# Kernel tuning notes

Measured on AMD Instinct MI355X. Metric: run time of the kernel, lower is better.

The kernel has to match this reference:

```python
import jax, jax.numpy as jnp
import numpy as np
from jax import lax

HID = 128


def setup_inputs() -> dict:
    key = jax.random.key(0)
    ks = jax.random.split(key, 14)
    B, T, D_IN, OUT, L = 256, 300, 700, 20, 4
    x = jax.random.normal(ks[0], (B, T, D_IN), jnp.float32)
    w_in = jax.random.normal(ks[1], (D_IN, HID), jnp.float32) / np.sqrt(D_IN).astype(np.float32)
    b_in = jnp.zeros((HID,), jnp.float32)
    A_w = jax.random.normal(ks[2], (L, HID, HID), jnp.float32) / np.sqrt(HID).astype(np.float32)
    # sparse recurrent mask: keep-prob 0.3 (dropout=0.7), no self-connections
    mask = (jax.random.uniform(ks[3], (L, HID, HID)) > 0.7).astype(jnp.float32) * (1.0 - jnp.eye(HID, dtype=jnp.float32))
    A_w = A_w * mask
    A_b = jax.random.normal(ks[4], (L, HID), jnp.float32) * 0.01
    fc_w = jax.random.normal(ks[5], (L, HID, HID), jnp.float32) / np.sqrt(HID).astype(np.float32)
    fc_b = jnp.zeros((L, HID), jnp.float32)
    w_out = jax.random.normal(ks[6], (L * HID, OUT), jnp.float32) / np.sqrt(L * HID).astype(np.float32)
    b_out = jnp.zeros((OUT,), jnp.float32)
    thr = jax.random.uniform(ks[7], (HID,), jnp.float32) * 0.5
    decay = jax.random.uniform(ks[8], (HID,), jnp.float32) * 0.5
    rst = jax.random.uniform(ks[9], (HID,), jnp.float32) * 0.05
    mem0 = jax.random.uniform(ks[10], (L, B, HID), jnp.float32) * 0.1  # torch uniform_(0, 0.1)
    return dict(x=x, w_in=w_in, b_in=b_in, A_w=A_w, A_b=A_b, fc_w=fc_w, fc_b=fc_b,
                w_out=w_out, b_out=b_out, thr=thr, decay=decay, rst=rst, mem0=mem0)


def reference(x, w_in, b_in, A_w, A_b, fc_w, fc_b, w_out, b_out, thr, decay, rst, mem0):
    B, T, _ = x.shape
    # fixed input projection (fc_in frozen in original) -> [B,T,HID]
    inp = jnp.einsum('btd,dh->bth', x, w_in) + b_in
    # parallel mode: each reservoir drive depends only on input_t -> precompute all timesteps
    xs = jnp.einsum('bth,lhk->ltbk', inp, A_w) + A_b[:, None, None, :]  # [L,T,B,HID]
    xs = xs.transpose(1, 0, 2, 3)  # [T,L,B,HID]

    def step(carry, x_t):
        mem, spk = carry
        mem = rst * spk + mem * decay * (1.0 - spk) + x_t
        spike = (mem - thr > 0).astype(mem.dtype)
        return (mem, spike), (mem, spike)

    spk0 = jnp.zeros_like(mem0)
    _, (mems, spks) = lax.scan(step, (mem0, spk0), xs)  # each [T,L,B,HID]

    rates = spks.mean(axis=0)  # [L,B,HID] == sum_spk / time_step
    outs = jax.nn.relu(jnp.einsum('lbh,lhk->lbk', rates, fc_w) + fc_b[:, None, :])
    cat = jnp.concatenate([outs[0], outs[1], outs[2], outs[3]], axis=1)  # [B,4*HID]
    out = cat @ w_out + b_out  # [B,OUT]

    hid4_mem = jnp.concatenate([mem0[3][:, None, :], mems[:, 3].transpose(1, 0, 2)], axis=1)  # [B,T+1,HID]
    hid4_spk = jnp.concatenate([jnp.zeros((B, 1, HID), x.dtype), spks[:, 3].transpose(1, 0, 2)], axis=1)
    A_norm = jnp.sum(jnp.abs(A_w))
    return out, hid4_mem, hid4_spk, A_norm
```

## Files before the change

kernel.cpp:

```cpp
#include <hip/hip_runtime.h>

#define HID_   128
#define BB_    256
#define TT_    300
#define DIN_   700
#define LL_    4
#define NOUT_  20
#define NROWS_ (BB_*TT_)

#define OUT_OFF   0
#define HMEM_OFF  5120
#define HSPK_OFF  (5120 + 256*301*128)
#define ANORM_OFF (5120 + 2*256*301*128)

typedef __attribute__((ext_vector_type(8))) short  bfrag;
typedef __attribute__((ext_vector_type(4))) float  f32x4;

__device__ __forceinline__ unsigned short f2bf(float f) {
    unsigned int u = __float_as_uint(f);
    return (unsigned short)((u + 0x7fffu + ((u >> 16) & 1u)) >> 16);
}
__device__ __forceinline__ float bf2f(unsigned short h) {
    return __uint_as_float(((unsigned int)h) << 16);
}
__device__ __forceinline__ void split2(float v, unsigned short& hi, unsigned short& lo) {
    hi = f2bf(v);
    lo = f2bf(v - bf2f(hi));
}

__global__ __launch_bounds__(256, 2)
void k1_mfma(const float* __restrict__ x, const float* __restrict__ w,
             const float* __restrict__ bin, float* __restrict__ inp)
{
    __shared__ unsigned short whi[128 * 40];
    __shared__ unsigned short wlo[128 * 40];

    const int tid  = threadIdx.x;
    const int wave = tid >> 6;
    const int lane = tid & 63;
    const int l15  = lane & 15;
    const int kg   = lane >> 4;
    const long m0  = (long)blockIdx.x * 64 + wave * 16;
    const long arow = m0 + l15;

    f32x4 acc[8];
#pragma unroll
    for (int nt = 0; nt < 8; ++nt) {
        const float bv = bin[nt * 16 + l15];
        acc[nt] = (f32x4){bv, bv, bv, bv};
    }

    for (int ks = 0; ks < 22; ++ks) {
        const int k0 = ks * 32;
        const int lim = (700 - k0) * 128;
        const float* __restrict__ wsrc = w + (long)k0 * 128;
#pragma unroll
        for (int j = 0; j < 16; ++j) {
            const int i = tid + j * 256;
            const int kk = i >> 7, nn = i & 127;
            float v = (i < lim) ? wsrc[i] : 0.f;
            unsigned short hi, lo;
            split2(v, hi, lo);
            whi[nn * 40 + kk] = hi;
            wlo[nn * 40 + kk] = lo;
        }
        __syncthreads();

        bfrag ahi, alo;
        const int kbase = k0 + kg * 8;
        const float* __restrict__ xr = x + arow * (long)DIN_ + kbase;
        if (kbase + 7 < 700) {
            const float4 p0 = *(const float4*)(xr);
            const float4 p1 = *(const float4*)(xr + 4);
            float vv[8] = {p0.x, p0.y, p0.z, p0.w, p1.x, p1.y, p1.z, p1.w};
#pragma unroll
            for (int j = 0; j < 8; ++j) {
                unsigned short hi, lo; split2(vv[j], hi, lo);
                ahi[j] = (short)hi; alo[j] = (short)lo;
            }
        } else {
#pragma unroll
            for (int j = 0; j < 8; ++j) {
                float v = (kbase + j < 700) ? xr[j] : 0.f;
                unsigned short hi, lo; split2(v, hi, lo);
                ahi[j] = (short)hi; alo[j] = (short)lo;
            }
        }

#pragma unroll
        for (int nt = 0; nt < 8; ++nt) {
            const int boff = (nt * 16 + l15) * 40 + kg * 8;
            const bfrag bhi = *(const bfrag*)&whi[boff];
            const bfrag blo = *(const bfrag*)&wlo[boff];
            acc[nt] = __builtin_amdgcn_mfma_f32_16x16x32_bf16(ahi, bhi, acc[nt], 0, 0, 0);
            acc[nt] = __builtin_amdgcn_mfma_f32_16x16x32_bf16(ahi, blo, acc[nt], 0, 0, 0);
            acc[nt] = __builtin_amdgcn_mfma_f32_16x16x32_bf16(alo, bhi, acc[nt], 0, 0, 0);
        }
        __syncthreads();
    }

#pragma unroll
    for (int nt = 0; nt < 8; ++nt) {
        const int col = nt * 16 + l15;
#pragma unroll
        for (int reg = 0; reg < 4; ++reg)
            inp[(m0 + kg * 4 + reg) * (long)HID_ + col] = acc[nt][reg];
    }
}

__global__ __launch_bounds__(256, 2)
void k2_mfma(const float* __restrict__ inp, const float* __restrict__ Aw,
             const float* __restrict__ Ab, float* __restrict__ xs,
             int lsel, long lstride)
{
    __shared__ unsigned short ahiS[128 * 72];
    __shared__ unsigned short aloS[128 * 72];

    const int tid  = threadIdx.x;
    const int wave = tid >> 6;
    const int lane = tid & 63;
    const int l15  = lane & 15;
    const int kg   = lane >> 4;
    const int l    = (lsel >= 0) ? lsel : (int)blockIdx.y;
    const long m0  = (long)blockIdx.x * 64 + wave * 16;
    const long arow = m0 + l15;
    const long lbase = (lsel >= 0) ? 0 : (long)l * lstride;

    f32x4 acc[8];
#pragma unroll
    for (int nt = 0; nt < 8; ++nt) {
        const float bv = Ab[l * 128 + nt * 16 + l15];
        acc[nt] = (f32x4){bv, bv, bv, bv};
    }

    const float* __restrict__ Al = Aw + (long)l * 128 * 128;

    for (int kc = 0; kc < 2; ++kc) {
        const float* __restrict__ asrc = Al + (long)kc * 64 * 128;
#pragma unroll
        for (int j = 0; j < 32; ++j) {
            const int i = tid + j * 256;
            const int kk = i >> 7, nn = i & 127;
            unsigned short hi, lo;
            split2(asrc[i], hi, lo);
            ahiS[nn * 72 + kk] = hi;
            aloS[nn * 72 + kk] = lo;
        }
        __syncthreads();

#pragma unroll
        for (int ks = 0; ks < 2; ++ks) {
            const int k0 = kc * 64 + ks * 32;
            bfrag ahi, alo;
            const float* __restrict__ ir = inp + arow * (long)HID_ + k0 + kg * 8;
            const float4 p0 = *(const float4*)(ir);
            const float4 p1 = *(const float4*)(ir + 4);
            float vv[8] = {p0.x, p0.y, p0.z, p0.w, p1.x, p1.y, p1.z, p1.w};
#pragma unroll
            for (int j = 0; j < 8; ++j) {
                unsigned short hi, lo; split2(vv[j], hi, lo);
                ahi[j] = (short)hi; alo[j] = (short)lo;
            }

#pragma unroll
            for (int nt = 0; nt < 8; ++nt) {
                const int boff = (nt * 16 + l15) * 72 + ks * 32 + kg * 8;
                const bfrag bhi = *(const bfrag*)&ahiS[boff];
                const bfrag blo = *(const bfrag*)&aloS[boff];
                acc[nt] = __builtin_amdgcn_mfma_f32_16x16x32_bf16(ahi, bhi, acc[nt], 0, 0, 0);
                acc[nt] = __builtin_amdgcn_mfma_f32_16x16x32_bf16(ahi, blo, acc[nt], 0, 0, 0);
                acc[nt] = __builtin_amdgcn_mfma_f32_16x16x32_bf16(alo, bhi, acc[nt], 0, 0, 0);
            }
        }
        __syncthreads();
    }

#pragma unroll
    for (int nt = 0; nt < 8; ++nt) {
        const int col = nt * 16 + l15;
#pragma unroll
        for (int reg = 0; reg < 4; ++reg)
            xs[(lbase + m0 + kg * 4 + reg) * (long)HID_ + col] = acc[nt][reg];
    }
}

__global__ __launch_bounds__(128, 4)
void k3_scan_split(const float* __restrict__ xs, const float* __restrict__ thr,
                   const float* __restrict__ dec, const float* __restrict__ rstv,
                   const float* __restrict__ mem0, float* __restrict__ rates,
                   float* __restrict__ omem, float* __restrict__ ospk,
                   int lsel, long lstride)
{
    const int h = threadIdx.x;
    int l, b;
    if (lsel >= 0) { l = lsel; b = blockIdx.x; }
    else           { l = blockIdx.x >> 8; b = blockIdx.x & 255; }

    const float th = thr[h];
    const float dc = dec[h];
    const float rs = rstv[h];

    float mem = mem0[((long)l * 256 + b) * 128 + h];
    float spk = 0.f;
    float cnt = 0.f;

    const bool last = (l == 3);
    float* __restrict__ om = omem + (long)b * 301 * 128 + h;
    float* __restrict__ os = ospk + (long)b * 301 * 128 + h;
    if (last) { om[0] = mem; os[0] = 0.f; }

    const float* __restrict__ p =
        xs + ((lsel >= 0 ? 0L : (long)l * lstride) + (long)b * TT_) * HID_ + h;

    for (int t0 = 0; t0 < TT_; t0 += 20) {
        float v[20];
#pragma unroll
        for (int j = 0; j < 20; ++j) v[j] = p[(long)(t0 + j) * HID_];
#pragma unroll
        for (int j = 0; j < 20; ++j) {
            mem = rs * spk + mem * dc * (1.f - spk) + v[j];
            spk = (mem - th > 0.f) ? 1.f : 0.f;
            cnt += spk;
            if (last) {
                om[(long)(t0 + j + 1) * 128] = mem;
                os[(long)(t0 + j + 1) * 128] = spk;
            }
        }
    }

    rates[((long)l * 256 + b) * 128 + h] = cnt * (1.f / 300.f);
}

__global__ __launch_bounds__(128, 2)
void k3_fused(const float* __restrict__ inp, const float* __restrict__ Aw,
              const float* __restrict__ Ab, const float* __restrict__ thr,
              const float* __restrict__ dec, const float* __restrict__ rstv,
              const float* __restrict__ mem0, float* __restrict__ rates,
              float* __restrict__ omem, float* __restrict__ ospk)
{
    const int h = threadIdx.x;
    const int l = blockIdx.x & 3;
    const int b = blockIdx.x >> 2;

    float a[128];
#pragma unroll
    for (int k = 0; k < 128; ++k)
        a[k] = Aw[((long)l * 128 + k) * 128 + h];

    const float ab = Ab[l * 128 + h];
    const float th = thr[h];
    const float dc = dec[h];
    const float rs = rstv[h];

    float mem = mem0[((long)l * 256 + b) * 128 + h];
    float spk = 0.f, cnt = 0.f;

    const bool last = (l == 3);
    float* __restrict__ om = omem + (long)b * 301 * 128 + h;
    float* __restrict__ os = ospk + (long)b * 301 * 128 + h;
    if (last) { om[0] = mem; os[0] = 0.f; }

    const float* __restrict__ ip = inp + (long)b * 300 * 128;

    for (int t = 0; t < 300; ++t) {
        float acc = ab;
#pragma unroll
        for (int k = 0; k < 128; ++k)
            acc = fmaf(ip[k], a[k], acc);
        ip += 128;
        mem = rs * spk + mem * dc * (1.f - spk) + acc;
        spk = (mem - th > 0.f) ? 1.f : 0.f;
        cnt += spk;
        if (last) {
            om[(long)(t + 1) * 128] = mem;
            os[(long)(t + 1) * 128] = spk;
        }
    }
    rates[((long)l * 256 + b) * 128 + h] = cnt * (1.f / 300.f);
}

__global__ __launch_bounds__(256)
void k4_head(const float* __restrict__ rates, const float* __restrict__ fcw,
             const float* __restrict__ fcb, const float* __restrict__ wout,
             const float* __restrict__ bout, float* __restrict__ out)
{
    __shared__ float cat[512];
    const int b = blockIdx.x;
    const int tid = threadIdx.x;

    for (int c = tid; c < 512; c += 256) {
        const int l = c >> 7;
        const int k = c & 127;
        float s = fcb[l * 128 + k];
        const float* __restrict__ rp = rates + ((long)l * 256 + b) * 128;
        const float* __restrict__ wp = fcw + (long)l * 128 * 128 + k;
#pragma unroll 8
        for (int hh = 0; hh < 128; ++hh)
            s = fmaf(rp[hh], wp[(long)hh * 128], s);
        cat[c] = s > 0.f ? s : 0.f;
    }
    __syncthreads();

    if (tid < NOUT_) {
        float s = bout[tid];
#pragma unroll 8
        for (int c = 0; c < 512; ++c)
            s = fmaf(cat[c], wout[(long)c * NOUT_ + tid], s);
        out[(long)b * NOUT_ + tid] = s;
    }
}

__global__ __launch_bounds__(256)
void k5_anorm(const float* __restrict__ Aw, float* __restrict__ out)
{
    __shared__ float red[256];
    const int tid = threadIdx.x;
    float s = 0.f;
    for (int i = tid; i < LL_ * 128 * 128; i += 256)
        s += fabsf(Aw[i]);
    red[tid] = s;
    __syncthreads();
#pragma unroll
    for (int st = 128; st > 0; st >>= 1) {
        if (tid < st) red[tid] += red[tid + st];
        __syncthreads();
    }
    if (tid == 0) out[0] = red[0];
}

extern "C" void kernel_launch(void* const* d_in, const int* in_sizes, int n_in,
                              void* d_out, int out_size, void* d_ws, size_t ws_size,
                              hipStream_t stream)
{
    const float* x    = (const float*)d_in[0];
    const float* w_in = (const float*)d_in[1];
    const float* b_in = (const float*)d_in[2];
    const float* A_w  = (const float*)d_in[3];
    const float* A_b  = (const float*)d_in[4];
    const float* fc_w = (const float*)d_in[5];
    const float* fc_b = (const float*)d_in[6];
    const float* w_out= (const float*)d_in[7];
    const float* b_out= (const float*)d_in[8];
    const float* thr  = (const float*)d_in[9];
    const float* dec  = (const float*)d_in[10];
    const float* rst  = (const float*)d_in[11];
    const float* mem0 = (const float*)d_in[12];

    float* out = (float*)d_out;
    float* ws  = (float*)d_ws;

    const long INP_ELTS = (long)NROWS_ * HID_;
    const long XS_FULL  = 4L * NROWS_ * HID_;
    const long RATES    = 4L * 256 * 128;

    float* inp = ws;

    k1_mfma<<<1200, 256, 0, stream>>>(x, w_in, b_in, inp);

    const size_t need_full = (size_t)(INP_ELTS + XS_FULL + RATES) * 4;
    const size_t need_perl = (size_t)(INP_ELTS + INP_ELTS + RATES) * 4;

    if (ws_size >= need_full) {
        float* xs    = ws + INP_ELTS;
        float* rates = xs + XS_FULL;
        k2_mfma<<<dim3(1200, 4), 256, 0, stream>>>(inp, A_w, A_b, xs, -1, (long)NROWS_);
        k3_scan_split<<<1024, 128, 0, stream>>>(xs, thr, dec, rst, mem0, rates,
                                                out + HMEM_OFF, out + HSPK_OFF,
                                                -1, (long)NROWS_);
        k4_head<<<256, 256, 0, stream>>>(rates, fc_w, fc_b, w_out, b_out, out + OUT_OFF);
    } else if (ws_size >= need_perl) {
        float* xs    = ws + INP_ELTS;
        float* rates = xs + INP_ELTS;
        for (int l = 0; l < 4; ++l) {
            k2_mfma<<<dim3(1200, 1), 256, 0, stream>>>(inp, A_w, A_b, xs, l, 0L);
            k3_scan_split<<<256, 128, 0, stream>>>(xs, thr, dec, rst, mem0, rates,
                                                   out + HMEM_OFF, out + HSPK_OFF,
                                                   l, 0L);
        }
        k4_head<<<256, 256, 0, stream>>>(rates, fc_w, fc_b, w_out, b_out, out + OUT_OFF);
    } else {
        float* rates = ws + INP_ELTS;
        k3_fused<<<1024, 128, 0, stream>>>(inp, A_w, A_b, thr, dec, rst, mem0,
                                           rates, out + HMEM_OFF, out + HSPK_OFF);
        k4_head<<<256, 256, 0, stream>>>(rates, fc_w, fc_b, w_out, b_out, out + OUT_OFF);
    }

    k5_anorm<<<1, 256, 0, stream>>>(A_w, out + ANORM_OFF);
}
```

Before: 738.8 us.

## Presplit weights into bf16 hi/lo fragment layout and use register-tiled GEMMs

Adds a prepass kernel that splits w_in and A_w into bf16 hi/lo pairs, stored in MFMA fragment order in the workspace. New input-projection and reservoir-drive kernels then read B fragments straight from global memory instead of staging and splitting them in LDS. Each wave now handles 32 rows, and the drive kernel loops over all four layers so each block reuses its input tile. The aim is to cut repeated weight splitting and LDS traffic, at the cost of an extra launch, more workspace, and heavier register pressure.

```diff
diff --git a/kernel.cpp b/kernel.cpp
--- a/kernel.cpp
+++ b/kernel.cpp
@@ -13,6 +13,10 @@
 #define HSPK_OFF  (5120 + 256*301*128)
 #define ANORM_OFF (5120 + 2*256*301*128)
 
+#define W1ELTS (22*4096)
+#define A2ELTS (4*4*4096)
+#define PRESPLIT_FLOATS ((2*W1ELTS + 2*A2ELTS)/2)
+
 typedef __attribute__((ext_vector_type(8))) short  bfrag;
 typedef __attribute__((ext_vector_type(4))) float  f32x4;
 
@@ -26,6 +30,175 @@
 __device__ __forceinline__ void split2(float v, unsigned short& hi, unsigned short& lo) {
     hi = f2bf(v);
     lo = f2bf(v - bf2f(hi));
+}
+
+__global__ __launch_bounds__(256)
+void k0_presplit(const float* __restrict__ w, const float* __restrict__ Aw,
+                 unsigned short* __restrict__ w1hi, unsigned short* __restrict__ w1lo,
+                 unsigned short* __restrict__ a2hi, unsigned short* __restrict__ a2lo)
+{
+    const int f = blockIdx.x * 256 + threadIdx.x;
+    if (f < W1ELTS) {
+        const int ks = f >> 12, r = f & 4095;
+        const int nt = r >> 9, l15 = (r >> 5) & 15, kk = r & 31;
+        const int k = ks * 32 + kk, n = nt * 16 + l15;
+        const float v = (k < DIN_) ? w[(long)k * HID_ + n] : 0.f;
+        unsigned short hi, lo; split2(v, hi, lo);
+        w1hi[f] = hi; w1lo[f] = lo;
+    } else {
+        const int g = f - W1ELTS;
+        const int l = g >> 14, r2 = g & 16383;
+        const int ks = r2 >> 12, r = r2 & 4095;
+        const int nt = r >> 9, l15 = (r >> 5) & 15, kk = r & 31;
+        const int k = ks * 32 + kk, n = nt * 16 + l15;
+        const float v = Aw[(long)l * 16384 + (long)k * HID_ + n];
+        unsigned short hi, lo; split2(v, hi, lo);
+        a2hi[g] = hi; a2lo[g] = lo;
+    }
+}
+
+__global__ __launch_bounds__(256, 2)
+void k1_reg(const float* __restrict__ x,
+            const unsigned short* __restrict__ whi,
+            const unsigned short* __restrict__ wlo,
+            const float* __restrict__ bin, float* __restrict__ inp)
+{
+    const int tid  = threadIdx.x;
+    const int wave = tid >> 6;
+    const int lane = tid & 63;
+    const int l15  = lane & 15;
+    const int kg   = lane >> 4;
+    const long m0  = (long)blockIdx.x * 128 + wave * 32;
+
+    f32x4 acc[2][8];
+#pragma unroll
+    for (int nt = 0; nt < 8; ++nt) {
+        const float bv = bin[nt * 16 + l15];
+        acc[0][nt] = (f32x4){bv, bv, bv, bv};
+        acc[1][nt] = (f32x4){bv, bv, bv, bv};
+    }
+
+    const int foff = l15 * 32 + kg * 8;
+
+    for (int ks = 0; ks < 22; ++ks) {
+        const int kbase = ks * 32 + kg * 8;
+
+        bfrag ahi[2], alo[2];
+#pragma unroll
+        for (int m = 0; m < 2; ++m) {
+            const float* __restrict__ xr = x + (m0 + m * 16 + l15) * (long)DIN_ + kbase;
+            if (kbase + 7 < DIN_) {
+                const float4 p0 = *(const float4*)(xr);
+                const float4 p1 = *(const float4*)(xr + 4);
+                float vv[8] = {p0.x, p0.y, p0.z, p0.w, p1.x, p1.y, p1.z, p1.w};
+#pragma unroll
+                for (int j = 0; j < 8; ++j) {
+                    unsigned short hi, lo; split2(vv[j], hi, lo);
+                    ahi[m][j] = (short)hi; alo[m][j] = (short)lo;
+                }
+            } else {
+#pragma unroll
+                for (int j = 0; j < 8; ++j) {
+                    float v = (kbase + j < DIN_) ? xr[j] : 0.f;
+                    unsigned short hi, lo; split2(v, hi, lo);
+                    ahi[m][j] = (short)hi; alo[m][j] = (short)lo;
+                }
+            }
+        }
+
+        const unsigned short* __restrict__ wh = whi + (long)ks * 4096 + foff;
+        const unsigned short* __restrict__ wl = wlo + (long)ks * 4096 + foff;
+#pragma unroll
+        for (int nt = 0; nt < 8; ++nt) {
+            const bfrag bhi = *(const bfrag*)(wh + nt * 512);
+            const bfrag blo = *(const bfrag*)(wl + nt * 512);
+#pragma unroll
+            for (int m = 0; m < 2; ++m) {
+                acc[m][nt] = __builtin_amdgcn_mfma_f32_16x16x32_bf16(ahi[m], bhi, acc[m][nt], 0, 0, 0);
+                acc[m][nt] = __builtin_amdgcn_mfma_f32_16x16x32_bf16(ahi[m], blo, acc[m][nt], 0, 0, 0);
+                acc[m][nt] = __builtin_amdgcn_mfma_f32_16x16x32_bf16(alo[m], bhi, acc[m][nt], 0, 0, 0);
+            }
+        }
+    }
+
+#pragma unroll
+    for (int m = 0; m < 2; ++m)
+#pragma unroll
+        for (int nt = 0; nt < 8; ++nt) {
+            const int col = nt * 16 + l15;
+#pragma unroll
+            for (int reg = 0; reg < 4; ++reg)
+                inp[(m0 + m * 16 + kg * 4 + reg) * (long)HID_ + col] = acc[m][nt][reg];
+        }
+}
+
+__global__ __launch_bounds__(256, 2)
+void k2_reg(const float* __restrict__ inp,
+            const unsigned short* __restrict__ ahiP,
+            const unsigned short* __restrict__ aloP,
+            const float* __restrict__ Ab, float* __restrict__ xs)
+{
+    const int tid  = threadIdx.x;
+    const int wave = tid >> 6;
+    const int lane = tid & 63;
+    const int l15  = lane & 15;
+    const int kg   = lane >> 4;
+    const long m0  = (long)blockIdx.x * 128 + wave * 32;
+    const int foff = l15 * 32 + kg * 8;
+
+    for (int l = 0; l < 4; ++l) {
+        f32x4 acc[2][8];
+#pragma unroll
+        for (int nt = 0; nt < 8; ++nt) {
+            const float bv = Ab[l * HID_ + nt * 16 + l15];
+            acc[0][nt] = (f32x4){bv, bv, bv, bv};
+            acc[1][nt] = (f32x4){bv, bv, bv, bv};
+        }
+
+        const unsigned short* __restrict__ ph = ahiP + (long)l * 16384;
+        const unsigned short* __restrict__ pl = aloP + (long)l * 16384;
+
+#pragma unroll
+        for (int ks = 0; ks < 4; ++ks) {
+            bfrag xhi[2], xlo[2];
+#pragma unroll
+            for (int m = 0; m < 2; ++m) {
+                const float* __restrict__ ir = inp + (m0 + m * 16 + l15) * (long)HID_ + ks * 32 + kg * 8;
+                const float4 p0 = *(const float4*)(ir);
+                const float4 p1 = *(const float4*)(ir + 4);
+                float vv[8] = {p0.x, p0.y, p0.z, p0.w, p1.x, p1.y, p1.z, p1.w};
+#pragma unroll
+                for (int j = 0; j < 8; ++j) {
+                    unsigned short hi, lo; split2(vv[j], hi, lo);
+                    xhi[m][j] = (short)hi; xlo[m][j] = (short)lo;
+                }
+            }
+
+            const unsigned short* __restrict__ bh = ph + ks * 4096 + foff;
+            const unsigned short* __restrict__ bl = pl + ks * 4096 + foff;
+#pragma unroll
+            for (int nt = 0; nt < 8; ++nt) {
+                const bfrag bhi = *(const bfrag*)(bh + nt * 512);
+                const bfrag blo = *(const bfrag*)(bl + nt * 512);
+#pragma unroll
+                for (int m = 0; m < 2; ++m) {
+                    acc[m][nt] = __builtin_amdgcn_mfma_f32_16x16x32_bf16(xhi[m], bhi, acc[m][nt], 0, 0, 0);
+                    acc[m][nt] = __builtin_amdgcn_mfma_f32_16x16x32_bf16(xhi[m], blo, acc[m][nt], 0, 0, 0);
+                    acc[m][nt] = __builtin_amdgcn_mfma_f32_16x16x32_bf16(xlo[m], bhi, acc[m][nt], 0, 0, 0);
+                }
+            }
+        }
+
+#pragma unroll
+        for (int m = 0; m < 2; ++m)
+#pragma unroll
+            for (int nt = 0; nt < 8; ++nt) {
+                const int col = nt * 16 + l15;
+#pragma unroll
+                for (int reg = 0; reg < 4; ++reg)
+                    xs[((long)l * NROWS_ + m0 + m * 16 + kg * 4 + reg) * (long)HID_ + col] = acc[m][nt][reg];
+            }
+    }
 }
 
 __global__ __launch_bounds__(256, 2)
@@ -353,24 +526,42 @@
     const long XS_FULL  = 4L * NROWS_ * HID_;
     const long RATES    = 4L * 256 * 128;
 
-    float* inp = ws;
-
-    k1_mfma<<<1200, 256, 0, stream>>>(x, w_in, b_in, inp);
-
+    const size_t need_v2   = (size_t)(PRESPLIT_FLOATS + INP_ELTS + XS_FULL + RATES) * 4;
     const size_t need_full = (size_t)(INP_ELTS + XS_FULL + RATES) * 4;
     const size_t need_perl = (size_t)(INP_ELTS + INP_ELTS + RATES) * 4;
 
-    if (ws_size >= need_full) {
+    if (ws_size >= need_v2) {
+        unsigned short* us   = (unsigned short*)ws;
+        unsigned short* w1hi = us;
+        unsigned short* w1lo = us + W1ELTS;
+        unsigned short* a2hi = us + 2 * W1ELTS;
+        unsigned short* a2lo = us + 2 * W1ELTS + A2ELTS;
+        float* inp   = ws + PRESPLIT_FLOATS;
+        float* xs    = inp + INP_ELTS;
+        float* rates = xs + XS_FULL;
+
+        k0_presplit<<<608, 256, 0, stream>>>(w_in, A_w, w1hi, w1lo, a2hi, a2lo);
+        k1_reg<<<600, 256, 0, stream>>>(x, w1hi, w1lo, b_in, inp);
+        k2_reg<<<600, 256, 0, stream>>>(inp, a2hi, a2lo, A_b, xs);
+        k3_scan_split<<<1024, 128, 0, stream>>>(xs, thr, dec, rst, mem0, rates,
+                                                out + HMEM_OFF, out + HSPK_OFF,
+                                                -1, (long)NROWS_);
+        k4_head<<<256, 256, 0, stream>>>(rates, fc_w, fc_b, w_out, b_out, out + OUT_OFF);
+    } else if (ws_size >= need_full) {
+        float* inp   = ws;
         float* xs    = ws + INP_ELTS;
         float* rates = xs + XS_FULL;
+        k1_mfma<<<1200, 256, 0, stream>>>(x, w_in, b_in, inp);
         k2_mfma<<<dim3(1200, 4), 256, 0, stream>>>(inp, A_w, A_b, xs, -1, (long)NROWS_);
         k3_scan_split<<<1024, 128, 0, stream>>>(xs, thr, dec, rst, mem0, rates,
                                                 out + HMEM_OFF, out + HSPK_OFF,
                                                 -1, (long)NROWS_);
         k4_head<<<256, 256, 0, stream>>>(rates, fc_w, fc_b, w_out, b_out, out + OUT_OFF);
     } else if (ws_size >= need_perl) {
+        float* inp   = ws;
         float* xs    = ws + INP_ELTS;
         float* rates = xs + INP_ELTS;
+        k1_mfma<<<1200, 256, 0, stream>>>(x, w_in, b_in, inp);
         for (int l = 0; l < 4; ++l) {
             k2_mfma<<<dim3(1200, 1), 256, 0, stream>>>(inp, A_w, A_b, xs, l, 0L);
             k3_scan_split<<<256, 128, 0, stream>>>(xs, thr, dec, rst, mem0, rates,
@@ -379,7 +570,9 @@
         }
         k4_head<<<256, 256, 0, stream>>>(rates, fc_w, fc_b, w_out, b_out, out + OUT_OFF);
     } else {
+        float* inp   = ws;
         float* rates = ws + INP_ELTS;
+        k1_mfma<<<1200, 256, 0, stream>>>(x, w_in, b_in, inp);
         k3_fused<<<1024, 128, 0, stream>>>(inp, A_w, A_b, thr, dec, rst, mem0,
                                            rates, out + HMEM_OFF, out + HSPK_OFF);
         k4_head<<<256, 256, 0, stream>>>(rates, fc_w, fc_b, w_out, b_out, out + OUT_OFF);
```

Measured after the change: 746.4 us. About the same (+1.0%).
